# Kernel tuning notes

Hardware: AMD Instinct MI355X
Metric: run time of the kernel (lower is better)

Reference implementation:

```python
import jax, jax.numpy as jnp
import numpy as np
from jax import lax

B, H, W, DIM = 64, 32, 32, 448
HEADS, DH, WS = 8, 28, 8
INNER = DH * HEADS            # 224
C2 = DIM // 2                 # 224 (spatial branch channels == inner_dim)
HALF = INNER // 2             # 112 per attention sub-branch
SEQ_L1 = WS * WS              # 64 tokens per window
SEQ_L2 = (256 // HEADS) ** 2 // SEQ_L1  # 16 == number of windows (32x32 map)
SCALE = DH ** -0.5


def setup_inputs() -> dict:
    key = jax.random.key(0)
    ks = jax.random.split(key, 18)
    def nrm(k, shape, s):
        return jax.random.normal(k, shape, jnp.float32) * s
    inp = {}
    inp["x"] = jax.random.normal(ks[0], (B, H, W, DIM), jnp.float32)
    # trunc_normal_(std=1) positional biases -> clipped normals
    inp["pos_emb1"] = jnp.clip(jax.random.normal(ks[1], (1, 1, HEADS // 2, SEQ_L1, SEQ_L1), jnp.float32), -2.0, 2.0)
    inp["pos_emb2"] = jnp.clip(jax.random.normal(ks[2], (1, 1, HEADS // 2, SEQ_L2, SEQ_L2), jnp.float32), -2.0, 2.0)
    # linear weights stored (in, out)
    inp["Wq"] = nrm(ks[3], (C2, INNER), 0.02)
    inp["Wkv"] = nrm(ks[4], (C2, 2 * INNER), 0.02)
    inp["Wout"] = nrm(ks[5], (INNER, DIM), 0.02)
    inp["bout"] = nrm(ks[6], (DIM,), 0.02)
    # 3D conv weights (O, I, D, Kh, Kw), fan-in = 224*27 -> std ~ 0.01
    for i, name in enumerate(["convr", "conv1", "conv2", "conv3"]):
        inp[name + "_w"] = nrm(ks[7 + 2 * i], (C2, C2, 3, 3, 3), 0.01)
        inp[name + "_b"] = nrm(ks[8 + 2 * i], (C2,), 0.01)
    return inp


def _conv3d(t, w, b):
    y = lax.conv_general_dilated(t, w, (1, 1, 1), [(1, 1)] * 3,
                                 dimension_numbers=("NCDHW", "OIDHW", "NCDHW"))
    return y + b[None, :, None, None, None]


def _window(t):
    # [b, H, W, c] -> [b, n_windows, ws*ws, c]
    b, h, w, c = t.shape
    t = t.reshape(b, h // WS, WS, w // WS, WS, c).transpose(0, 1, 3, 2, 4, 5)
    return t.reshape(b, (h // WS) * (w // WS), WS * WS, c)


def _unwindow(t):
    # [b, n_windows, ws*ws, c] -> [b, H, W, c]
    b, n, m, c = t.shape
    t = t.reshape(b, H // WS, W // WS, WS, WS, c).transpose(0, 1, 3, 2, 4, 5)
    return t.reshape(b, H, W, c)


def _split_heads(t):
    # [b, n, m, half] -> [b, n, heads//2, m, dh]
    b, n, m, c = t.shape
    return t.reshape(b, n, m, HEADS // 2, DH).transpose(0, 1, 3, 2, 4)


def _merge_heads(t):
    # [b, n, heads//2, m, dh] -> [b, n, m, half]
    b, n, h, m, d = t.shape
    return t.transpose(0, 1, 3, 2, 4).reshape(b, n, m, h * d)


def _attn(q, q_, k, v, pos):
    del q_
    sim = jnp.einsum("bnhid,bnhjd->bnhij", q * SCALE, k) + pos
    a = jax.nn.softmax(sim, axis=-1)
    return jnp.einsum("bnhij,bnhjd->bnhid", a, v)


def reference(x, pos_emb1, pos_emb2, Wq, Wkv, Wout, bout,
              convr_w, convr_b, conv1_w, conv1_b, conv2_w, conv2_b, conv3_w, conv3_b):
    b = x.shape[0]
    x1 = x[..., :C2]
    x2 = x[..., C2:]
    # spectral 3D conv branch: [b, c2, 1, H, W]
    x2 = x2.transpose(0, 3, 1, 2)[:, :, None]
    res = jax.nn.relu(_conv3d(x2, convr_w, convr_b))
    o = jax.nn.relu(_conv3d(x2, conv1_w, conv1_b))
    o = jax.nn.relu(_conv3d(o, conv2_w, conv2_b))
    o = jax.nn.relu(_conv3d(o, conv3_w, conv3_b))
    X2S = (o + res)[:, :, 0].transpose(0, 2, 3, 1)  # [b, H, W, c2]

    q = x1 @ Wq
    kv = x1 @ Wkv
    k, v = kv[..., :INNER], kv[..., INNER:]
    q1, q2 = q[..., :HALF], q[..., HALF:]
    k1, k2 = k[..., :HALF], k[..., HALF:]
    v1, v2 = v[..., :HALF], v[..., HALF:]

    # local (within-window) branch
    q1h, k1h, v1h = map(lambda t: _split_heads(_window(t)), (q1, k1, v1))
    sim1 = jnp.einsum("bnhid,bnhjd->bnhij", q1h * SCALE, k1h) + pos_emb1
    out1 = jnp.einsum("bnhij,bnhjd->bnhid", jax.nn.softmax(sim1, axis=-1), v1h)
    out1 = _merge_heads(out1)  # [b, n, m, half]

    # grid (across-window) branch: swap window/token axes
    q2h, k2h, v2h = map(lambda t: _split_heads(_window(t).transpose(0, 2, 1, 3)), (q2, k2, v2))
    sim2 = jnp.einsum("bnhid,bnhjd->bnhij", q2h * SCALE, k2h) + pos_emb2
    out2 = jnp.einsum("bnhij,bnhjd->bnhid", jax.nn.softmax(sim2, axis=-1), v2h)
    out2 = _merge_heads(out2).transpose(0, 2, 1, 3)  # [b, n, m, half]

    out = jnp.concatenate([out1, out2], axis=-1) @ Wout + bout  # [b, n, m, DIM]
    out = _unwindow(out)
    return jnp.concatenate([out, X2S], axis=-1)  # [b, H, W, DIM + C2]
```

## Files before the change

### kernel.cpp

```cpp
#include <hip/hip_runtime.h>

typedef unsigned short u16;
typedef unsigned int   u32;
typedef __attribute__((ext_vector_type(4))) float  f32x4;
typedef __attribute__((ext_vector_type(8))) short  s16x8;
typedef __attribute__((ext_vector_type(8))) __bf16 bf16x8;
typedef __attribute__((ext_vector_type(2))) u32    u32x2;

#define DEV __device__ __forceinline__
#define SCALE_Q 0.1889822365046136f

DEV float bf2f(u16 u){ u32 x = ((u32)u)<<16; float f; __builtin_memcpy(&f,&x,4); return f; }
DEV u16   f2bf(float f){ u32 x; __builtin_memcpy(&x,&f,4); return (u16)((x + 0x7fffu + ((x>>16)&1u))>>16); }

DEV s16x8 cvt8(const float* __restrict__ src){
  f32x4 f0 = *(const f32x4*)src, f1 = *(const f32x4*)(src+4);
  bf16x8 b;
  b[0]=(__bf16)f0[0]; b[1]=(__bf16)f0[1]; b[2]=(__bf16)f0[2]; b[3]=(__bf16)f0[3];
  b[4]=(__bf16)f1[0]; b[5]=(__bf16)f1[1]; b[6]=(__bf16)f1[2]; b[7]=(__bf16)f1[3];
  return __builtin_bit_cast(s16x8, b);
}

DEV void gll16(const u16* g, u16* l){
  __builtin_amdgcn_global_load_lds(
      (const __attribute__((address_space(1))) u32*)(const void*)g,
      (__attribute__((address_space(3))) u32*)(void*)l,
      16, 0, 0);
}

DEV void ld28(const u16* __restrict__ p, float* dst, float scale){
#pragma unroll
  for (int j=0;j<7;j++){
    u32x2 w = *(const u32x2*)(p + j*4);
    dst[j*4+0] = bf2f((u16)(w[0]&0xffffu))*scale;
    dst[j*4+1] = bf2f((u16)(w[0]>>16))*scale;
    dst[j*4+2] = bf2f((u16)(w[1]&0xffffu))*scale;
    dst[j*4+3] = bf2f((u16)(w[1]>>16))*scale;
  }
}

__global__ void pack_k(const float* __restrict__ Wq, const float* __restrict__ Wkv,
                       const float* __restrict__ Wout,
                       const float* __restrict__ wr, const float* __restrict__ w1,
                       const float* __restrict__ w2, const float* __restrict__ w3,
                       u16* __restrict__ WqkvT, u16* __restrict__ WoutT,
                       u16* __restrict__ convW)
{
  int idx = blockIdx.x*256 + threadIdx.x;
  if (idx < 150528) {
    int nn = idx/224, k = idx - nn*224;
    float v;
    if (nn < 224)      v = Wq [k*224 + nn];
    else if (nn < 448) v = Wkv[k*448 + (nn-224)];
    else               v = Wkv[k*448 + (nn-448) + 224];
    WqkvT[idx] = f2bf(v);
  } else if (idx < 250880) {
    int j = idx - 150528;
    int nn = j/224, k = j - nn*224;
    WoutT[j] = f2bf(Wout[k*448 + nn]);
  } else {
    int j = idx - 250880;
    int cv = j/451584, rem = j - cv*451584;
    int co = rem/2016, kk = rem - co*2016;
    int tap = kk/224, ci = kk - tap*224;
    const float* w = (cv==0)?wr:(cv==1)?w1:(cv==2)?w2:w3;
    convW[j] = f2bf(w[(co*224 + ci)*27 + 9 + tap]);
  }
}

__global__ void prep_k(const float* __restrict__ x, u16* __restrict__ x1bf,
                       u16* __restrict__ xpad, u16* __restrict__ oApad,
                       u16* __restrict__ oBpad)
{
  int idx = blockIdx.x*256 + threadIdx.x;
  int pp = idx/28, c8 = idx - pp*28;
  int b = pp/1156, rem = pp - b*1156, y = rem/34, xx = rem - y*34;
  int c0 = c8*8;
  if (y>=1 && y<=32 && xx>=1 && xx<=32){
    int p = (b*32 + y-1)*32 + (xx-1);
    *(s16x8*)(x1bf + p*224 + c0) = cvt8(x + p*448 + c0);
    *(s16x8*)(xpad + pp*224 + c0) = cvt8(x + p*448 + 224 + c0);
  } else {
    const s16x8 z = {0,0,0,0,0,0,0,0};
    *(s16x8*)(xpad  + pp*224 + c0) = z;
    *(s16x8*)(oApad + pp*224 + c0) = z;
    *(s16x8*)(oBpad + pp*224 + c0) = z;
  }
}

enum { M_FUSED=0, M_C2=1, M_C3=2, M_QKV=3, M_OUT=4 };

template<int MODE>
__global__ __launch_bounds__(512,4) void gemm_k(
    const u16* __restrict__ A, const u16* __restrict__ Bt,
    const float* __restrict__ bias0, const float* __restrict__ bias1,
    u16* __restrict__ outA, u16* __restrict__ outB, float* __restrict__ outF)
{
  constexpr bool CONV = (MODE==M_FUSED || MODE==M_C2 || MODE==M_C3);
  constexpr int KTOT = CONV ? 2016 : 224;
  constexpr int KS   = KTOT/32;

  __shared__ __align__(16) u16 Als[2][128*32];
  __shared__ __align__(16) u16 Bls[2][224*32];

  const int t  = threadIdx.x;
  const int bmRaw = blockIdx.x, nb = blockIdx.y;
  const int bm = ((bmRaw&7)<<6) + (bmRaw>>3);
  const int lane = t&63, lr = lane&15, lg = lane>>4;
  const int w = t>>6, wm = w>>1, wn = w&1;

  const int arow = t>>2;
  const int qsrc = ((t&3) - ((t>>4)&3)) & 3;
  const int acol8 = qsrc*8;
  const int p0 = bm*128 + arow;
  int PP0 = 0;
  if constexpr (CONV) PP0 = ((p0>>10)*34 + ((p0>>5)&31) + 1)*34 + (p0&31) + 1;
  const int Bb0 = (nb*224 +       arow)*KTOT + acol8;
  const int Bb1 = (nb*224 + 128 + arow)*KTOT + acol8;

  u16* aBase[2] = { &Als[0][0] + w*512, &Als[1][0] + w*512 };
  u16* bBase[2] = { &Bls[0][0] + w*512, &Bls[1][0] + w*512 };

  auto STAGE = [&](int buf, int ks){
    if constexpr (CONV){
      const int kc  = ks/9;
      const int tap = ks - kc*9;
      const int ty = tap/3, tx = tap - ty*3;
      const int toff = (ty-1)*34 + (tx-1);
      const int koff = tap*224 + kc*32;
      gll16(A + (PP0+toff)*224 + kc*32 + acol8, aBase[buf]);
      gll16(Bt + Bb0 + koff, bBase[buf]);
      if (w < 6) gll16(Bt + Bb1 + koff, bBase[buf] + 4096);
    } else {
      gll16(A + p0*224 + ks*32 + acol8, aBase[buf]);
      gll16(Bt + Bb0 + ks*32, bBase[buf]);
      if (w < 6) gll16(Bt + Bb1 + ks*32, bBase[buf] + 4096);
    }
  };

  f32x4 acc[2][7];
  { f32x4 zf = {0.f,0.f,0.f,0.f};
#pragma unroll
    for (int i=0;i<2;i++)
#pragma unroll
      for (int j=0;j<7;j++) acc[i][j] = zf; }

  STAGE(0, 0);
  __syncthreads();

  for (int ks=0; ks<KS; ++ks){
    const int cur = ks&1;
    if (ks+1 < KS) STAGE(cur^1, ks+1);

    const u16* Ac = &Als[cur][0];
    const u16* Bc = &Bls[cur][0];
    bf16x8 af[2], bfv[7];
#pragma unroll
    for (int mi=0; mi<2; ++mi){
      const int row = wm*32 + mi*16 + lr;
      af[mi] = *(const bf16x8*)(Ac + row*32 + ((lg + (row>>2))&3)*8);
    }
#pragma unroll
    for (int ni=0; ni<7; ++ni){
      const int row = wn*112 + ni*16 + lr;
      bfv[ni] = *(const bf16x8*)(Bc + row*32 + ((lg + (row>>2))&3)*8);
    }

#pragma unroll
    for (int ni=0; ni<7; ++ni)
#pragma unroll
      for (int mi=0; mi<2; ++mi)
        acc[mi][ni] = __builtin_amdgcn_mfma_f32_16x16x32_bf16(af[mi], bfv[ni], acc[mi][ni], 0,0,0);

    __syncthreads();
  }

  const float* bs;
  if constexpr (MODE==M_FUSED) bs = (nb==0) ? bias0 : bias1;
  else bs = bias0;

#pragma unroll
  for (int mi=0; mi<2; ++mi){
    const int rbase = bm*128 + wm*32 + mi*16 + lg*4;
#pragma unroll
    for (int ni=0; ni<7; ++ni){
      const int col = wn*112 + ni*16 + lr;
#pragma unroll
      for (int r=0;r<4;r++){
        const int row = rbase + r;
        float v = acc[mi][ni][r];
        if constexpr (MODE==M_FUSED){
          v = fmaxf(v + bs[col], 0.f);
          if (nb==0){
            outF[row*672 + 448 + col] = v;
          } else {
            const int pp = ((row>>10)*34 + ((row>>5)&31) + 1)*34 + (row&31) + 1;
            outB[pp*224 + col] = f2bf(v);
          }
        } else if constexpr (MODE==M_C2){
          v = fmaxf(v + bs[col], 0.f);
          const int pp = ((row>>10)*34 + ((row>>5)&31) + 1)*34 + (row&31) + 1;
          outB[pp*224 + col] = f2bf(v);
        } else if constexpr (MODE==M_C3){
          v = fmaxf(v + bs[col], 0.f);
          const int o = row*672 + 448 + col;
          outF[o] = v + outF[o];
        } else if constexpr (MODE==M_QKV){
          outA[row*672 + nb*224 + col] = f2bf(v);
        } else {
          outF[row*672 + nb*224 + col] = v + bs[nb*224 + col];
        }
      }
    }
  }
}

__global__ __launch_bounds__(256,2) void attn1_k(const u16* __restrict__ qkv,
    const float* __restrict__ pos1, u16* __restrict__ attnout)
{
  __shared__ __align__(16) float KL[64][112];
  __shared__ __align__(16) float VL[64][112];
  const int t = threadIdx.x;
  const int b = blockIdx.x>>4, n = blockIdx.x&15;
  const int base = b*1024 + (n>>2)*256 + (n&3)*8;
  {
    const int r = t>>2, part = t&3;
    const int pr_ = base + (r>>3)*32 + (r&7);
    const u16* kp = qkv + pr_*672 + 224 + part*28;
    const u16* vp = kp + 224;
#pragma unroll
    for (int j=0;j<7;j++){
      u32x2 kk = *(const u32x2*)(kp + j*4);
      u32x2 vv = *(const u32x2*)(vp + j*4);
      const int c = part*28 + j*4;
      KL[r][c+0]=bf2f((u16)(kk[0]&0xffffu)); KL[r][c+1]=bf2f((u16)(kk[0]>>16));
      KL[r][c+2]=bf2f((u16)(kk[1]&0xffffu)); KL[r][c+3]=bf2f((u16)(kk[1]>>16));
      VL[r][c+0]=bf2f((u16)(vv[0]&0xffffu)); VL[r][c+1]=bf2f((u16)(vv[0]>>16));
      VL[r][c+2]=bf2f((u16)(vv[1]&0xffffu)); VL[r][c+3]=bf2f((u16)(vv[1]>>16));
    }
  }
  __syncthreads();

  const int h = t>>6, i = t&63;
  const int pi = base + (i>>3)*32 + (i&7);
  float q[28];
  ld28(qkv + pi*672 + h*28, q, SCALE_Q);

  float s[64];
  const float* pr = pos1 + (h*64+i)*64;
#pragma unroll
  for (int j4=0;j4<16;j4++){
    f32x4 pv = *(const f32x4*)(pr + j4*4);
    s[j4*4+0]=pv[0]; s[j4*4+1]=pv[1]; s[j4*4+2]=pv[2]; s[j4*4+3]=pv[3];
  }
  const int c0 = h*28;
#pragma unroll
  for (int j=0;j<64;j++){
    const f32x4* kr = (const f32x4*)&KL[j][c0];
    float a0=0.f,a1=0.f,a2=0.f,a3=0.f;
#pragma unroll
    for (int u=0;u<7;u++){
      f32x4 kv = kr[u];
      a0 += q[u*4+0]*kv[0]; a1 += q[u*4+1]*kv[1];
      a2 += q[u*4+2]*kv[2]; a3 += q[u*4+3]*kv[3];
    }
    s[j] += (a0+a1)+(a2+a3);
  }
  float mx = s[0];
#pragma unroll
  for (int j=1;j<64;j++) mx = fmaxf(mx, s[j]);
  float sum = 0.f;
#pragma unroll
  for (int j=0;j<64;j++){ float e = __expf(s[j]-mx); s[j]=e; sum+=e; }
  const float inv = 1.f/sum;

  float out[28];
#pragma unroll
  for (int u=0;u<28;u++) out[u]=0.f;
#pragma unroll
  for (int j=0;j<64;j++){
    const float pj = s[j];
    const f32x4* vr = (const f32x4*)&VL[j][c0];
#pragma unroll
    for (int u=0;u<7;u++){
      f32x4 vv = vr[u];
      out[u*4+0] += pj*vv[0]; out[u*4+1] += pj*vv[1];
      out[u*4+2] += pj*vv[2]; out[u*4+3] += pj*vv[3];
    }
  }
  u16* op = attnout + pi*224 + h*28;
#pragma unroll
  for (int u=0;u<7;u++){
    u32x2 wv;
    wv[0] = (u32)f2bf(out[u*4+0]*inv) | ((u32)f2bf(out[u*4+1]*inv)<<16);
    wv[1] = (u32)f2bf(out[u*4+2]*inv) | ((u32)f2bf(out[u*4+3]*inv)<<16);
    *(u32x2*)(op + u*4) = wv;
  }
}

__global__ __launch_bounds__(256,1) void attn2_k(const u16* __restrict__ qkv,
    const float* __restrict__ pos2, u16* __restrict__ attnout)
{
  const int t = threadIdx.x;
  const int b = blockIdx.x>>4, mg = blockIdx.x&15;
  const int m = mg*4 + (t>>6);
  const int lane = t&63, h = lane>>4, i = lane&15;
  const int base = b*1024 + (m>>3)*32 + (m&7);
  const int pi = base + (i>>2)*256 + (i&3)*8;

  float q[28];
  ld28(qkv + pi*672 + 112 + h*28, q, SCALE_Q);

  float s[16];
  const float* pr = pos2 + (h*16+i)*16;
#pragma unroll
  for (int j4=0;j4<4;j4++){
    f32x4 pv = *(const f32x4*)(pr + j4*4);
    s[j4*4+0]=pv[0]; s[j4*4+1]=pv[1]; s[j4*4+2]=pv[2]; s[j4*4+3]=pv[3];
  }
#pragma unroll
  for (int j=0;j<16;j++){
    const int pj_ = base + (j>>2)*256 + (j&3)*8;
    float kk[28];
    ld28(qkv + pj_*672 + 336 + h*28, kk, 1.0f);
    float a=0.f;
#pragma unroll
    for (int u=0;u<28;u++) a += q[u]*kk[u];
    s[j] += a;
  }
  float mx = s[0];
#pragma unroll
  for (int j=1;j<16;j++) mx = fmaxf(mx, s[j]);
  float sum = 0.f;
#pragma unroll
  for (int j=0;j<16;j++){ float e = __expf(s[j]-mx); s[j]=e; sum+=e; }
  const float inv = 1.f/sum;

  float out[28];
#pragma unroll
  for (int u=0;u<28;u++) out[u]=0.f;
#pragma unroll
  for (int j=0;j<16;j++){
    const int pj_ = base + (j>>2)*256 + (j&3)*8;
    float vv[28];
    ld28(qkv + pj_*672 + 560 + h*28, vv, 1.0f);
    const float pj = s[j];
#pragma unroll
    for (int u=0;u<28;u++) out[u] += pj*vv[u];
  }
  u16* op = attnout + pi*224 + 112 + h*28;
#pragma unroll
  for (int u=0;u<7;u++){
    u32x2 wv;
    wv[0] = (u32)f2bf(out[u*4+0]*inv) | ((u32)f2bf(out[u*4+1]*inv)<<16);
    wv[1] = (u32)f2bf(out[u*4+2]*inv) | ((u32)f2bf(out[u*4+3]*inv)<<16);
    *(u32x2*)(op + u*4) = wv;
  }
}

extern "C" void kernel_launch(void* const* d_in, const int* in_sizes, int n_in,
                              void* d_out, int out_size, void* d_ws, size_t ws_size,
                              hipStream_t stream) {
  const float* x    = (const float*)d_in[0];
  const float* pos1 = (const float*)d_in[1];
  const float* pos2 = (const float*)d_in[2];
  const float* Wq   = (const float*)d_in[3];
  const float* Wkv  = (const float*)d_in[4];
  const float* Wout = (const float*)d_in[5];
  const float* bout = (const float*)d_in[6];
  const float* wr   = (const float*)d_in[7];
  const float* br   = (const float*)d_in[8];
  const float* w1   = (const float*)d_in[9];
  const float* b1   = (const float*)d_in[10];
  const float* w2   = (const float*)d_in[11];
  const float* b2   = (const float*)d_in[12];
  const float* w3   = (const float*)d_in[13];
  const float* b3   = (const float*)d_in[14];

  char* ws = (char*)d_ws;
  const size_t PADSZ = 73984ull*224*2;
  const size_t FLATS = 65536ull*224*2;
  u16* xpad   = (u16*)(ws);
  u16* oApad  = (u16*)(ws + PADSZ);
  u16* oBpad  = (u16*)(ws + 2*PADSZ);
  u16* x1bf   = (u16*)(ws + 3*PADSZ);
  u16* convW  = (u16*)(ws + 3*PADSZ + FLATS);
  u16* WqkvT  = convW + 4*451584;
  u16* WoutT  = WqkvT + 672*224;
  u16* qkv     = (u16*)(ws);
  u16* attnout = (u16*)(ws + 88080384);
  float* dout  = (float*)d_out;

  pack_k<<<8036, 256, 0, stream>>>(Wq, Wkv, Wout, wr, w1, w2, w3, WqkvT, WoutT, convW);
  prep_k<<<8092, 256, 0, stream>>>(x, x1bf, xpad, oApad, oBpad);

  gemm_k<M_FUSED><<<dim3(512,2), 512, 0, stream>>>(xpad,  convW,          br, b1, nullptr, oApad, dout);
  gemm_k<M_C2  ><<<dim3(512,1), 512, 0, stream>>>(oApad, convW+2*451584, b2, nullptr, nullptr, oBpad, nullptr);
  gemm_k<M_C3  ><<<dim3(512,1), 512, 0, stream>>>(oBpad, convW+3*451584, b3, nullptr, nullptr, nullptr, dout);

  gemm_k<M_QKV ><<<dim3(512,3), 512, 0, stream>>>(x1bf, WqkvT, nullptr, nullptr, qkv, nullptr, nullptr);
  attn1_k<<<1024, 256, 0, stream>>>(qkv, pos1, attnout);
  attn2_k<<<1024, 256, 0, stream>>>(qkv, pos2, attnout);
  gemm_k<M_OUT ><<<dim3(512,2), 512, 0, stream>>>(attnout, WoutT, bout, nullptr, nullptr, nullptr, dout);
}
```

Baseline: 510.6 us.

## Triple-buffer GEMM LDS staging with two-ahead prefetch and vmcnt-based waits

Replaces the double-buffered LDS pipeline with a three-stage ring, issuing global-to-LDS loads two K-steps ahead. Full __syncthreads are replaced by partial s_waitcnt vmcnt plus raw barriers, and the MFMA block is wrapped in s_setprio. Every wave now loads B rows, with out-of-range rows clamped to row 223, so the load count stays uniform for vmcnt accounting. This is meant to hide global memory latency, at the cost of more LDS per block (which may reduce occupancy under launch_bounds 512,4) and redundant B loads.

New measurement: 564.3 us. 1.11x slower.

```diff
diff --git a/kernel.cpp b/kernel.cpp
--- a/kernel.cpp
+++ b/kernel.cpp
@@ -100,8 +100,8 @@
   constexpr int KTOT = CONV ? 2016 : 224;
   constexpr int KS   = KTOT/32;
 
-  __shared__ __align__(16) u16 Als[2][128*32];
-  __shared__ __align__(16) u16 Bls[2][224*32];
+  __shared__ __align__(16) u16 AlsF[3*128*32];
+  __shared__ __align__(16) u16 BlsF[3*256*32];
 
   const int t  = threadIdx.x;
   const int bmRaw = blockIdx.x, nb = blockIdx.y;
@@ -115,27 +115,32 @@
   const int p0 = bm*128 + arow;
   int PP0 = 0;
   if constexpr (CONV) PP0 = ((p0>>10)*34 + ((p0>>5)&31) + 1)*34 + (p0&31) + 1;
-  const int Bb0 = (nb*224 +       arow)*KTOT + acol8;
-  const int Bb1 = (nb*224 + 128 + arow)*KTOT + acol8;
-
-  u16* aBase[2] = { &Als[0][0] + w*512, &Als[1][0] + w*512 };
-  u16* bBase[2] = { &Bls[0][0] + w*512, &Bls[1][0] + w*512 };
+  const int srow1 = (128 + arow > 223) ? 223 : (128 + arow);
+  const int Bb0 = (nb*224 + arow )*KTOT + acol8;
+  const int Bb1 = (nb*224 + srow1)*KTOT + acol8;
+
+  u16* aW = &AlsF[0] + w*512;
+  u16* bW = &BlsF[0] + w*512;
 
   auto STAGE = [&](int buf, int ks){
+    const u16 *asrc, *b0src, *b1src;
     if constexpr (CONV){
       const int kc  = ks/9;
       const int tap = ks - kc*9;
       const int ty = tap/3, tx = tap - ty*3;
       const int toff = (ty-1)*34 + (tx-1);
       const int koff = tap*224 + kc*32;
-      gll16(A + (PP0+toff)*224 + kc*32 + acol8, aBase[buf]);
-      gll16(Bt + Bb0 + koff, bBase[buf]);
-      if (w < 6) gll16(Bt + Bb1 + koff, bBase[buf] + 4096);
+      asrc  = A  + (PP0+toff)*224 + kc*32 + acol8;
+      b0src = Bt + Bb0 + koff;
+      b1src = Bt + Bb1 + koff;
     } else {
-      gll16(A + p0*224 + ks*32 + acol8, aBase[buf]);
-      gll16(Bt + Bb0 + ks*32, bBase[buf]);
-      if (w < 6) gll16(Bt + Bb1 + ks*32, bBase[buf] + 4096);
-    }
+      asrc  = A  + p0*224 + ks*32 + acol8;
+      b0src = Bt + Bb0 + ks*32;
+      b1src = Bt + Bb1 + ks*32;
+    }
+    gll16(asrc,  aW + buf*4096);
+    gll16(b0src, bW + buf*8192);
+    gll16(b1src, bW + buf*8192 + 4096);
   };
 
   f32x4 acc[2][7];
@@ -146,14 +151,20 @@
       for (int j=0;j<7;j++) acc[i][j] = zf; }
 
   STAGE(0, 0);
-  __syncthreads();
-
+  STAGE(1, 1);
+  asm volatile("s_waitcnt vmcnt(3)" ::: "memory");
+  __builtin_amdgcn_s_barrier();
+  __builtin_amdgcn_sched_barrier(0);
+
+  int cur = 0;
   for (int ks=0; ks<KS; ++ks){
-    const int cur = ks&1;
-    if (ks+1 < KS) STAGE(cur^1, ks+1);
-
-    const u16* Ac = &Als[cur][0];
-    const u16* Bc = &Bls[cur][0];
+    if (ks+2 < KS){
+      int nb3 = cur+2; if (nb3>=3) nb3-=3;
+      STAGE(nb3, ks+2);
+    }
+
+    const u16* Ac = &AlsF[0] + cur*4096;
+    const u16* Bc = &BlsF[0] + cur*8192;
     bf16x8 af[2], bfv[7];
 #pragma unroll
     for (int mi=0; mi<2; ++mi){
@@ -166,13 +177,21 @@
       bfv[ni] = *(const bf16x8*)(Bc + row*32 + ((lg + (row>>2))&3)*8);
     }
 
+    __builtin_amdgcn_s_setprio(1);
 #pragma unroll
     for (int ni=0; ni<7; ++ni)
 #pragma unroll
       for (int mi=0; mi<2; ++mi)
         acc[mi][ni] = __builtin_amdgcn_mfma_f32_16x16x32_bf16(af[mi], bfv[ni], acc[mi][ni], 0,0,0);
-
-    __syncthreads();
+    __builtin_amdgcn_s_setprio(0);
+
+    if (ks < KS-1){
+      if (ks == KS-2) asm volatile("s_waitcnt vmcnt(0)" ::: "memory");
+      else            asm volatile("s_waitcnt vmcnt(3)" ::: "memory");
+      __builtin_amdgcn_s_barrier();
+      __builtin_amdgcn_sched_barrier(0);
+    }
+    cur = (cur==2) ? 0 : cur+1;
   }
 
   const float* bs;
```

## Triple-buffer GEMM LDS staging with split-phase loads, barriers and MFMA priority

Applied to the files above, without the earlier changes.

Moves the GEMM main loop from double to triple buffering in LDS, prefetching two k-steps ahead. Each step is split into two halves, with A/B0 loads issued in the first and B1 in the second, and explicit vmcnt waits and raw s_barrier replace __syncthreads. MFMA blocks are wrapped in s_setprio so waves reach the matrix cores sooner. The goal is to hide global-to-LDS latency. In exchange it needs more LDS per block, which may lower occupancy under launch_bounds(512,4), and it clamps the B1 rows for all waves, which adds redundant loads.

After: 538.2 us. 5.4% more time.

```diff
diff --git a/kernel.cpp b/kernel.cpp
--- a/kernel.cpp
+++ b/kernel.cpp
@@ -100,8 +100,8 @@
   constexpr int KTOT = CONV ? 2016 : 224;
   constexpr int KS   = KTOT/32;
 
-  __shared__ __align__(16) u16 Als[2][128*32];
-  __shared__ __align__(16) u16 Bls[2][224*32];
+  __shared__ __align__(16) u16 Als[3][128*32];
+  __shared__ __align__(16) u16 Bls[3][256*32];
 
   const int t  = threadIdx.x;
   const int bmRaw = blockIdx.x, nb = blockIdx.y;
@@ -115,28 +115,30 @@
   const int p0 = bm*128 + arow;
   int PP0 = 0;
   if constexpr (CONV) PP0 = ((p0>>10)*34 + ((p0>>5)&31) + 1)*34 + (p0&31) + 1;
-  const int Bb0 = (nb*224 +       arow)*KTOT + acol8;
-  const int Bb1 = (nb*224 + 128 + arow)*KTOT + acol8;
-
-  u16* aBase[2] = { &Als[0][0] + w*512, &Als[1][0] + w*512 };
-  u16* bBase[2] = { &Bls[0][0] + w*512, &Bls[1][0] + w*512 };
-
-  auto STAGE = [&](int buf, int ks){
+  const int brow1 = (128 + arow > 223) ? 223 : (128 + arow);
+  const int Bb0 = (nb*224 + arow )*KTOT + acol8;
+  const int Bb1 = (nb*224 + brow1)*KTOT + acol8;
+
+  auto koffA = [&](int ks)->int{
     if constexpr (CONV){
-      const int kc  = ks/9;
-      const int tap = ks - kc*9;
+      const int kc = ks/9, tap = ks - kc*9;
       const int ty = tap/3, tx = tap - ty*3;
-      const int toff = (ty-1)*34 + (tx-1);
-      const int koff = tap*224 + kc*32;
-      gll16(A + (PP0+toff)*224 + kc*32 + acol8, aBase[buf]);
-      gll16(Bt + Bb0 + koff, bBase[buf]);
-      if (w < 6) gll16(Bt + Bb1 + koff, bBase[buf] + 4096);
-    } else {
-      gll16(A + p0*224 + ks*32 + acol8, aBase[buf]);
-      gll16(Bt + Bb0 + ks*32, bBase[buf]);
-      if (w < 6) gll16(Bt + Bb1 + ks*32, bBase[buf] + 4096);
-    }
+      return ((ty-1)*34 + (tx-1))*224 + kc*32;
+    } else return ks*32;
   };
+  auto koffB = [&](int ks)->int{
+    if constexpr (CONV){
+      const int kc = ks/9, tap = ks - kc*9;
+      return tap*224 + kc*32;
+    } else return ks*32;
+  };
+
+  auto STAGE_A  = [&](int buf, int ks){
+    if constexpr (CONV) gll16(A + PP0*224 + koffA(ks) + acol8, &Als[buf][0] + w*512);
+    else                gll16(A + p0*224  + koffA(ks) + acol8, &Als[buf][0] + w*512);
+  };
+  auto STAGE_B0 = [&](int buf, int ks){ gll16(Bt + Bb0 + koffB(ks), &Bls[buf][0] + w*512); };
+  auto STAGE_B1 = [&](int buf, int ks){ gll16(Bt + Bb1 + koffB(ks), &Bls[buf][0] + 4096 + w*512); };
 
   f32x4 acc[2][7];
   { f32x4 zf = {0.f,0.f,0.f,0.f};
@@ -145,34 +147,63 @@
 #pragma unroll
       for (int j=0;j<7;j++) acc[i][j] = zf; }
 
-  STAGE(0, 0);
-  __syncthreads();
-
+  STAGE_A(0,0); STAGE_B0(0,0); STAGE_B1(0,0);
+  STAGE_A(1,1); STAGE_B0(1,1); STAGE_B1(1,1);
+  asm volatile("s_waitcnt vmcnt(3)" ::: "memory");
+  __builtin_amdgcn_s_barrier();
+
+  const int arA0 = wm*32 +      lr;
+  const int arA1 = wm*32 + 16 + lr;
+  const int cA0 = ((lg + (arA0>>2))&3)*8;
+  const int cA1 = ((lg + (arA1>>2))&3)*8;
+
+  int cur = 0;
   for (int ks=0; ks<KS; ++ks){
-    const int cur = ks&1;
-    if (ks+1 < KS) STAGE(cur^1, ks+1);
-
+    int n2 = cur+2; if (n2>=3) n2-=3;
     const u16* Ac = &Als[cur][0];
     const u16* Bc = &Bls[cur][0];
-    bf16x8 af[2], bfv[7];
-#pragma unroll
-    for (int mi=0; mi<2; ++mi){
-      const int row = wm*32 + mi*16 + lr;
-      af[mi] = *(const bf16x8*)(Ac + row*32 + ((lg + (row>>2))&3)*8);
-    }
-#pragma unroll
-    for (int ni=0; ni<7; ++ni){
+
+    bf16x8 af0 = *(const bf16x8*)(Ac + arA0*32 + cA0);
+    bf16x8 af1 = *(const bf16x8*)(Ac + arA1*32 + cA1);
+    bf16x8 bfv[7];
+#pragma unroll
+    for (int ni=0; ni<4; ++ni){
       const int row = wn*112 + ni*16 + lr;
       bfv[ni] = *(const bf16x8*)(Bc + row*32 + ((lg + (row>>2))&3)*8);
     }
-
-#pragma unroll
-    for (int ni=0; ni<7; ++ni)
-#pragma unroll
-      for (int mi=0; mi<2; ++mi)
-        acc[mi][ni] = __builtin_amdgcn_mfma_f32_16x16x32_bf16(af[mi], bfv[ni], acc[mi][ni], 0,0,0);
-
-    __syncthreads();
+    if (ks+2 < KS){ STAGE_A(n2, ks+2); STAGE_B0(n2, ks+2); }
+    asm volatile("" ::: "memory");
+    __builtin_amdgcn_s_barrier();
+
+    __builtin_amdgcn_s_setprio(1);
+#pragma unroll
+    for (int ni=0; ni<4; ++ni){
+      acc[0][ni] = __builtin_amdgcn_mfma_f32_16x16x32_bf16(af0, bfv[ni], acc[0][ni], 0,0,0);
+      acc[1][ni] = __builtin_amdgcn_mfma_f32_16x16x32_bf16(af1, bfv[ni], acc[1][ni], 0,0,0);
+    }
+    __builtin_amdgcn_s_setprio(0);
+
+#pragma unroll
+    for (int ni=4; ni<7; ++ni){
+      const int row = wn*112 + ni*16 + lr;
+      bfv[ni] = *(const bf16x8*)(Bc + row*32 + ((lg + (row>>2))&3)*8);
+    }
+    if (ks+2 < KS) STAGE_B1(n2, ks+2);
+    asm volatile("" ::: "memory");
+    __builtin_amdgcn_s_barrier();
+
+    __builtin_amdgcn_s_setprio(1);
+#pragma unroll
+    for (int ni=4; ni<7; ++ni){
+      acc[0][ni] = __builtin_amdgcn_mfma_f32_16x16x32_bf16(af0, bfv[ni], acc[0][ni], 0,0,0);
+      acc[1][ni] = __builtin_amdgcn_mfma_f32_16x16x32_bf16(af1, bfv[ni], acc[1][ni], 0,0,0);
+    }
+    __builtin_amdgcn_s_setprio(0);
+
+    if (ks == KS-2) asm volatile("s_waitcnt vmcnt(0)" ::: "memory");
+    else            asm volatile("s_waitcnt vmcnt(3)" ::: "memory");
+    __builtin_amdgcn_s_barrier();
+    cur = (cur==2) ? 0 : cur+1;
   }
 
   const float* bs;
```

## Co-schedule independent GEMMs and attention branches in merged launches

Applied to the files above, without the earlier changes.

Merges independent work into shared launches: the first conv GEMM runs together with the QKV projection, conv3 together with the output projection, and both attention branches share one kernel. This needs a larger workspace layout so qkv no longer aliases xpad. The conv K-loop is also restructured into nested channel-chunk and tap loops so tap offsets are computed at compile time instead of with a runtime divide. The intent is to fill the GPU better and cut launch and tail gaps. The cost is a heavier per-block code path and a fallback branch for small workspaces. attn2 now runs under attn1's launch bounds and LDS allocation, which may change its occupancy.

New measurement: 554.4 us. 8.6% more time.

```diff
diff --git a/kernel.cpp b/kernel.cpp
--- a/kernel.cpp
+++ b/kernel.cpp
@@ -91,7 +91,7 @@
 enum { M_FUSED=0, M_C2=1, M_C3=2, M_QKV=3, M_OUT=4 };
 
 template<int MODE>
-__global__ __launch_bounds__(512,4) void gemm_k(
+DEV void gemm_body(u16* __restrict__ lds, int bmRaw, int nb,
     const u16* __restrict__ A, const u16* __restrict__ Bt,
     const float* __restrict__ bias0, const float* __restrict__ bias1,
     u16* __restrict__ outA, u16* __restrict__ outB, float* __restrict__ outF)
@@ -100,11 +100,7 @@
   constexpr int KTOT = CONV ? 2016 : 224;
   constexpr int KS   = KTOT/32;
 
-  __shared__ __align__(16) u16 Als[2][128*32];
-  __shared__ __align__(16) u16 Bls[2][224*32];
-
   const int t  = threadIdx.x;
-  const int bmRaw = blockIdx.x, nb = blockIdx.y;
   const int bm = ((bmRaw&7)<<6) + (bmRaw>>3);
   const int lane = t&63, lr = lane&15, lg = lane>>4;
   const int w = t>>6, wm = w>>1, wn = w&1;
@@ -118,24 +114,13 @@
   const int Bb0 = (nb*224 +       arow)*KTOT + acol8;
   const int Bb1 = (nb*224 + 128 + arow)*KTOT + acol8;
 
-  u16* aBase[2] = { &Als[0][0] + w*512, &Als[1][0] + w*512 };
-  u16* bBase[2] = { &Bls[0][0] + w*512, &Bls[1][0] + w*512 };
-
-  auto STAGE = [&](int buf, int ks){
-    if constexpr (CONV){
-      const int kc  = ks/9;
-      const int tap = ks - kc*9;
-      const int ty = tap/3, tx = tap - ty*3;
-      const int toff = (ty-1)*34 + (tx-1);
-      const int koff = tap*224 + kc*32;
-      gll16(A + (PP0+toff)*224 + kc*32 + acol8, aBase[buf]);
-      gll16(Bt + Bb0 + koff, bBase[buf]);
-      if (w < 6) gll16(Bt + Bb1 + koff, bBase[buf] + 4096);
-    } else {
-      gll16(A + p0*224 + ks*32 + acol8, aBase[buf]);
-      gll16(Bt + Bb0 + ks*32, bBase[buf]);
-      if (w < 6) gll16(Bt + Bb1 + ks*32, bBase[buf] + 4096);
-    }
+  u16* aW = lds + w*512;
+  u16* bW = lds + 8192 + w*512;
+
+  auto STAGE = [&](int buf, int aoff, int boff){
+    gll16(A + aoff, aW + buf*4096);
+    gll16(Bt + Bb0 + boff, bW + buf*7168);
+    if (w < 6) gll16(Bt + Bb1 + boff, bW + buf*7168 + 4096);
   };
 
   f32x4 acc[2][7];
@@ -145,34 +130,55 @@
 #pragma unroll
       for (int j=0;j<7;j++) acc[i][j] = zf; }
 
-  STAGE(0, 0);
-  __syncthreads();
-
-  for (int ks=0; ks<KS; ++ks){
-    const int cur = ks&1;
-    if (ks+1 < KS) STAGE(cur^1, ks+1);
-
-    const u16* Ac = &Als[cur][0];
-    const u16* Bc = &Bls[cur][0];
-    bf16x8 af[2], bfv[7];
-#pragma unroll
-    for (int mi=0; mi<2; ++mi){
-      const int row = wm*32 + mi*16 + lr;
-      af[mi] = *(const bf16x8*)(Ac + row*32 + ((lg + (row>>2))&3)*8);
-    }
+  const int rA0 = wm*32 + lr, rA1 = rA0 + 16;
+  const int cA0 = ((lg + (rA0>>2))&3)*8, cA1 = ((lg + (rA1>>2))&3)*8;
+
+  auto COMPUTE = [&](int cur){
+    const u16* Ac = lds + cur*4096;
+    const u16* Bc = lds + 8192 + cur*7168;
+    bf16x8 af0 = *(const bf16x8*)(Ac + rA0*32 + cA0);
+    bf16x8 af1 = *(const bf16x8*)(Ac + rA1*32 + cA1);
+    bf16x8 bfv[7];
 #pragma unroll
     for (int ni=0; ni<7; ++ni){
       const int row = wn*112 + ni*16 + lr;
       bfv[ni] = *(const bf16x8*)(Bc + row*32 + ((lg + (row>>2))&3)*8);
     }
-
-#pragma unroll
-    for (int ni=0; ni<7; ++ni)
-#pragma unroll
-      for (int mi=0; mi<2; ++mi)
-        acc[mi][ni] = __builtin_amdgcn_mfma_f32_16x16x32_bf16(af[mi], bfv[ni], acc[mi][ni], 0,0,0);
-
+#pragma unroll
+    for (int ni=0; ni<7; ++ni){
+      acc[0][ni] = __builtin_amdgcn_mfma_f32_16x16x32_bf16(af0, bfv[ni], acc[0][ni], 0,0,0);
+      acc[1][ni] = __builtin_amdgcn_mfma_f32_16x16x32_bf16(af1, bfv[ni], acc[1][ni], 0,0,0);
+    }
+  };
+
+  if constexpr (CONV){
+    STAGE(0, (PP0-35)*224 + acol8, 0);
     __syncthreads();
+    int cur = 0;
+    for (int kc=0; kc<7; ++kc){
+#pragma unroll
+      for (int tap=0; tap<9; ++tap){
+        if (kc*9 + tap + 1 < KS){
+          const int tapn = (tap+1)%9;
+          const int kcn  = kc + (tap==8 ? 1:0);
+          const int tyn  = tapn/3, txn = tapn - tyn*3;
+          const int toffn = (tyn-1)*34 + (txn-1);
+          STAGE(cur^1, (PP0+toffn)*224 + kcn*32 + acol8, tapn*224 + kcn*32);
+        }
+        COMPUTE(cur);
+        __syncthreads();
+        cur ^= 1;
+      }
+    }
+  } else {
+    STAGE(0, p0*224 + acol8, 0);
+    __syncthreads();
+    for (int ks=0; ks<KS; ++ks){
+      const int cur = ks&1;
+      if (ks+1 < KS) STAGE(cur^1, p0*224 + (ks+1)*32 + acol8, (ks+1)*32);
+      COMPUTE(cur);
+      __syncthreads();
+    }
   }
 
   const float* bs;
@@ -215,13 +221,38 @@
   }
 }
 
-__global__ __launch_bounds__(256,2) void attn1_k(const u16* __restrict__ qkv,
-    const float* __restrict__ pos1, u16* __restrict__ attnout)
-{
-  __shared__ __align__(16) float KL[64][112];
-  __shared__ __align__(16) float VL[64][112];
+template<int MODE>
+__global__ __launch_bounds__(512,4) void gemm_k(
+    const u16* __restrict__ A, const u16* __restrict__ Bt,
+    const float* __restrict__ bias0, const float* __restrict__ bias1,
+    u16* __restrict__ outA, u16* __restrict__ outB, float* __restrict__ outF)
+{
+  __shared__ __align__(16) u16 lds[22528];
+  gemm_body<MODE>(lds, blockIdx.x, blockIdx.y, A, Bt, bias0, bias1, outA, outB, outF);
+}
+
+template<int MA, int NBA, int MB>
+__global__ __launch_bounds__(512,4) void gemm_pair_k(
+    const u16* __restrict__ Aa, const u16* __restrict__ Bta,
+    const float* __restrict__ b0a, const float* __restrict__ b1a,
+    u16* __restrict__ oAa, u16* __restrict__ oBa, float* __restrict__ oFa,
+    const u16* __restrict__ Ab, const u16* __restrict__ Btb,
+    const float* __restrict__ b0b,
+    u16* __restrict__ oAb, u16* __restrict__ oBb, float* __restrict__ oFb)
+{
+  __shared__ __align__(16) u16 lds[22528];
+  if ((int)blockIdx.y < NBA)
+    gemm_body<MA>(lds, blockIdx.x, blockIdx.y, Aa, Bta, b0a, b1a, oAa, oBa, oFa);
+  else
+    gemm_body<MB>(lds, blockIdx.x, (int)blockIdx.y - NBA, Ab, Btb, b0b, nullptr, oAb, oBb, oFb);
+}
+
+DEV void attn1_body(float (*KL)[112], float (*VL)[112],
+                    const u16* __restrict__ qkv, const float* __restrict__ pos1,
+                    u16* __restrict__ attnout, int blk)
+{
   const int t = threadIdx.x;
-  const int b = blockIdx.x>>4, n = blockIdx.x&15;
+  const int b = blk>>4, n = blk&15;
   const int base = b*1024 + (n>>2)*256 + (n&3)*8;
   {
     const int r = t>>2, part = t&3;
@@ -298,11 +329,11 @@
   }
 }
 
-__global__ __launch_bounds__(256,1) void attn2_k(const u16* __restrict__ qkv,
-    const float* __restrict__ pos2, u16* __restrict__ attnout)
+DEV void attn2_body(const u16* __restrict__ qkv, const float* __restrict__ pos2,
+                    u16* __restrict__ attnout, int blk)
 {
   const int t = threadIdx.x;
-  const int b = blockIdx.x>>4, mg = blockIdx.x&15;
+  const int b = blk>>4, mg = blk&15;
   const int m = mg*4 + (t>>6);
   const int lane = t&63, h = lane>>4, i = lane&15;
   const int base = b*1024 + (m>>3)*32 + (m&7);
@@ -356,6 +387,16 @@
     wv[1] = (u32)f2bf(out[u*4+2]*inv) | ((u32)f2bf(out[u*4+3]*inv)<<16);
     *(u32x2*)(op + u*4) = wv;
   }
+}
+
+__global__ __launch_bounds__(256,2) void attn12_k(const u16* __restrict__ qkv,
+    const float* __restrict__ pos1, const float* __restrict__ pos2,
+    u16* __restrict__ attnout)
+{
+  __shared__ __align__(16) float KL[64][112];
+  __shared__ __align__(16) float VL[64][112];
+  if (blockIdx.x < 1024) attn1_body(KL, VL, qkv, pos1, attnout, blockIdx.x);
+  else                   attn2_body(qkv, pos2, attnout, blockIdx.x - 1024);
 }
 
 extern "C" void kernel_launch(void* const* d_in, const int* in_sizes, int n_in,
@@ -380,26 +421,54 @@
   char* ws = (char*)d_ws;
   const size_t PADSZ = 73984ull*224*2;
   const size_t FLATS = 65536ull*224*2;
-  u16* xpad   = (u16*)(ws);
-  u16* oApad  = (u16*)(ws + PADSZ);
-  u16* oBpad  = (u16*)(ws + 2*PADSZ);
-  u16* x1bf   = (u16*)(ws + 3*PADSZ);
-  u16* convW  = (u16*)(ws + 3*PADSZ + FLATS);
-  u16* WqkvT  = convW + 4*451584;
-  u16* WoutT  = WqkvT + 672*224;
-  u16* qkv     = (u16*)(ws);
-  u16* attnout = (u16*)(ws + 88080384);
-  float* dout  = (float*)d_out;
-
-  pack_k<<<8036, 256, 0, stream>>>(Wq, Wkv, Wout, wr, w1, w2, w3, WqkvT, WoutT, convW);
-  prep_k<<<8092, 256, 0, stream>>>(x, x1bf, xpad, oApad, oBpad);
-
-  gemm_k<M_FUSED><<<dim3(512,2), 512, 0, stream>>>(xpad,  convW,          br, b1, nullptr, oApad, dout);
-  gemm_k<M_C2  ><<<dim3(512,1), 512, 0, stream>>>(oApad, convW+2*451584, b2, nullptr, nullptr, oBpad, nullptr);
-  gemm_k<M_C3  ><<<dim3(512,1), 512, 0, stream>>>(oBpad, convW+3*451584, b3, nullptr, nullptr, nullptr, dout);
-
-  gemm_k<M_QKV ><<<dim3(512,3), 512, 0, stream>>>(x1bf, WqkvT, nullptr, nullptr, qkv, nullptr, nullptr);
-  attn1_k<<<1024, 256, 0, stream>>>(qkv, pos1, attnout);
-  attn2_k<<<1024, 256, 0, stream>>>(qkv, pos2, attnout);
-  gemm_k<M_OUT ><<<dim3(512,2), 512, 0, stream>>>(attnout, WoutT, bout, nullptr, nullptr, nullptr, dout);
-}
+  const size_t QKVSZ = 65536ull*672*2;
+  const size_t WTSZ  = 2057216ull*2;
+  float* dout = (float*)d_out;
+
+  const bool bigws = (ws_size >= FLATS + 3*PADSZ + QKVSZ + WTSZ);
+
+  if (bigws){
+    u16* x1bf    = (u16*)(ws);
+    u16* xpad    = (u16*)(ws + FLATS);
+    u16* oApad   = (u16*)(ws + FLATS + PADSZ);
+    u16* oBpad   = (u16*)(ws + FLATS + 2*PADSZ);
+    u16* qkv     = (u16*)(ws + FLATS + 3*PADSZ);
+    u16* convW   = (u16*)(ws + FLATS + 3*PADSZ + QKVSZ);
+    u16* WqkvT   = convW + 4*451584;
+    u16* WoutT   = WqkvT + 672*224;
+    u16* attnout = xpad;
+
+    pack_k<<<8036, 256, 0, stream>>>(Wq, Wkv, Wout, wr, w1, w2, w3, WqkvT, WoutT, convW);
+    prep_k<<<8092, 256, 0, stream>>>(x, x1bf, xpad, oApad, oBpad);
+
+    gemm_pair_k<M_FUSED,2,M_QKV><<<dim3(512,5), 512, 0, stream>>>(
+        xpad, convW, br, b1, nullptr, oApad, dout,
+        x1bf, WqkvT, nullptr, qkv, nullptr, nullptr);
+    gemm_k<M_C2><<<dim3(512,1), 512, 0, stream>>>(oApad, convW+2*451584, b2, nullptr, nullptr, oBpad, nullptr);
+    attn12_k<<<2048, 256, 0, stream>>>(qkv, pos1, pos2, attnout);
+    gemm_pair_k<M_C3,1,M_OUT><<<dim3(512,3), 512, 0, stream>>>(
+        oBpad, convW+3*451584, b3, nullptr, nullptr, nullptr, dout,
+        attnout, WoutT, bout, nullptr, nullptr, dout);
+  } else {
+    u16* xpad    = (u16*)(ws);
+    u16* oApad   = (u16*)(ws + PADSZ);
+    u16* oBpad   = (u16*)(ws + 2*PADSZ);
+    u16* x1bf    = (u16*)(ws + 3*PADSZ);
+    u16* convW   = (u16*)(ws + 3*PADSZ + FLATS);
+    u16* WqkvT   = convW + 4*451584;
+    u16* WoutT   = WqkvT + 672*224;
+    u16* qkv     = (u16*)(ws);
+    u16* attnout = (u16*)(ws + 88080384);
+
+    pack_k<<<8036, 256, 0, stream>>>(Wq, Wkv, Wout, wr, w1, w2, w3, WqkvT, WoutT, convW);
+    prep_k<<<8092, 256, 0, stream>>>(x, x1bf, xpad, oApad, oBpad);
+
+    gemm_k<M_FUSED><<<dim3(512,2), 512, 0, stream>>>(xpad,  convW,          br, b1, nullptr, oApad, dout);
+    gemm_k<M_C2  ><<<dim3(512,1), 512, 0, stream>>>(oApad, convW+2*451584, b2, nullptr, nullptr, oBpad, nullptr);
+    gemm_k<M_C3  ><<<dim3(512,1), 512, 0, stream>>>(oBpad, convW+3*451584, b3, nullptr, nullptr, nullptr, dout);
+
+    gemm_k<M_QKV ><<<dim3(512,3), 512, 0, stream>>>(x1bf, WqkvT, nullptr, nullptr, qkv, nullptr, nullptr);
+    attn12_k<<<2048, 256, 0, stream>>>(qkv, pos1, pos2, attnout);
+    gemm_k<M_OUT ><<<dim3(512,2), 512, 0, stream>>>(attnout, WoutT, bout, nullptr, nullptr, nullptr, dout);
+  }
+}
```
